# Kernel optimization log

Hardware: AMD Instinct MI355X
Metric: run time of the kernel (lower is better)

## Reference

```python
import jax, jax.numpy as jnp
import numpy as np

C = 256
CI = C // 2  # inter_channel = 128
B, H, W = 8, 64, 64


def setup_inputs() -> dict:
    key = jax.random.key(0)
    ks = jax.random.split(key, 9)
    s = 0.02
    return {
        "x": jax.random.normal(ks[0], (B, C, H, W), jnp.float32),
        "w_phi": jax.random.normal(ks[1], (CI, C), jnp.float32) * s,
        "b_phi": jax.random.normal(ks[2], (CI,), jnp.float32) * s,
        "w_theta": jax.random.normal(ks[3], (CI, C), jnp.float32) * s,
        "b_theta": jax.random.normal(ks[4], (CI,), jnp.float32) * s,
        "w_g": jax.random.normal(ks[5], (CI, C), jnp.float32) * s,
        "b_g": jax.random.normal(ks[6], (CI,), jnp.float32) * s,
        "w_mask": jax.random.normal(ks[7], (C, CI), jnp.float32) * s,
        "b_mask": jax.random.normal(ks[8], (C,), jnp.float32) * s,
    }


def reference(x, w_phi, b_phi, w_theta, b_theta, w_g, b_g, w_mask, b_mask):
    b, c, h, w = x.shape
    n = h * w
    xf = x.reshape(b, c, n)  # [b, c, n]
    # 1x1 convs == per-position channel projections
    phi = jnp.einsum('dc,bcn->bdn', w_phi, xf) + b_phi[:, None]      # [b, ci, n]
    theta = jnp.einsum('dc,bcn->bnd', w_theta, xf) + b_theta[None, None, :]  # [b, n, ci]
    g = jnp.einsum('dc,bcn->bnd', w_g, xf) + b_g[None, None, :]      # [b, n, ci]
    # full self-attention over spatial positions (no scaling, as in source)
    scores = jnp.einsum('bnd,bdm->bnm', theta, phi)                  # [b, n, n]
    attn = jax.nn.softmax(scores, axis=-1)
    y = jnp.einsum('bnm,bmd->bnd', attn, g)                          # [b, n, ci]
    # mask conv (1x1) back to channel dim + residual
    mask = jnp.einsum('cd,bnd->bcn', w_mask, y) + b_mask[:, None]    # [b, c, n]
    return mask.reshape(b, c, h, w) + x
```

## Files before the change

### kernel.cpp

```cpp
#include <hip/hip_runtime.h>

#define BB 8
#define CC 256
#define DD 128
#define NN 4096

#define LOG2E 1.44269504f
#define MSHIFT 32.0f

typedef __attribute__((ext_vector_type(8))) short short8;
typedef __attribute__((ext_vector_type(4))) short short4v;
typedef __attribute__((ext_vector_type(4))) float f32x4;
typedef __attribute__((ext_vector_type(16))) float f32x16;
typedef __attribute__((ext_vector_type(4))) unsigned int u32x4;

static __device__ __forceinline__ unsigned short f2bf(float f) {
    unsigned u = __builtin_bit_cast(unsigned, f);
    u += 0x7FFFu + ((u >> 16) & 1u);
    return (unsigned short)(u >> 16);
}
static __device__ __forceinline__ float bf2f(unsigned short h) {
    unsigned u = ((unsigned)h) << 16;
    return __builtin_bit_cast(float, u);
}
static __device__ __forceinline__ short8 pack8(float4 a, float4 b) {
    short8 r;
    r[0] = (short)f2bf(a.x); r[1] = (short)f2bf(a.y);
    r[2] = (short)f2bf(a.z); r[3] = (short)f2bf(a.w);
    r[4] = (short)f2bf(b.x); r[5] = (short)f2bf(b.y);
    r[6] = (short)f2bf(b.z); r[7] = (short)f2bf(b.w);
    return r;
}
static __device__ __forceinline__ unsigned cvtpk_bf16(float lo, float hi) {
    unsigned r;
    asm("v_cvt_pk_bf16_f32 %0, %1, %2" : "=v"(r) : "v"(lo), "v"(hi));
    return r;
}
static __device__ __forceinline__ void pl32swap(unsigned &a, unsigned &b) {
#if __has_builtin(__builtin_amdgcn_permlane32_swap)
    auto r = __builtin_amdgcn_permlane32_swap((int)a, (int)b, false, false);
    a = (unsigned)r[0]; b = (unsigned)r[1];
#else
    asm("v_permlane32_swap_b32 %0, %1" : "+v"(a), "+v"(b));
#endif
}

__global__ __launch_bounds__(256) void k_transpose_x(
        const float* __restrict__ x, unsigned short* __restrict__ xT) {
    __shared__ __align__(16) unsigned short tile[64][66];
    int nb = blockIdx.x * 64, cb = blockIdx.y * 64, b = blockIdx.z;
    const float* xp = x + (size_t)b * CC * NN;
    int t = threadIdx.x;
#pragma unroll
    for (int i = 0; i < 2; i++) {
        int idx = t + 256 * i;
        int c_l = idx >> 3;
        int n0 = (idx & 7) * 8;
        const float* src = xp + (size_t)(cb + c_l) * NN + nb + n0;
        float4 v0 = *(const float4*)(src);
        float4 v1 = *(const float4*)(src + 4);
        tile[n0 + 0][c_l] = f2bf(v0.x);
        tile[n0 + 1][c_l] = f2bf(v0.y);
        tile[n0 + 2][c_l] = f2bf(v0.z);
        tile[n0 + 3][c_l] = f2bf(v0.w);
        tile[n0 + 4][c_l] = f2bf(v1.x);
        tile[n0 + 5][c_l] = f2bf(v1.y);
        tile[n0 + 6][c_l] = f2bf(v1.z);
        tile[n0 + 7][c_l] = f2bf(v1.w);
    }
    __syncthreads();
    unsigned short* xtp = xT + (size_t)b * NN * CC;
#pragma unroll
    for (int i = 0; i < 2; i++) {
        int idx = t + 256 * i;
        int n_l = idx >> 3;
        int c0 = (idx & 7) * 8;
        const unsigned int* row = (const unsigned int*)&tile[n_l][0];
        uint4 o;
        o.x = row[(c0 >> 1) + 0];
        o.y = row[(c0 >> 1) + 1];
        o.z = row[(c0 >> 1) + 2];
        o.w = row[(c0 >> 1) + 3];
        *(uint4*)(xtp + (size_t)(nb + n_l) * CC + cb + c0) = o;
    }
}

__global__ __launch_bounds__(256) void k_proj(
        const unsigned short* __restrict__ xT,
        const float* __restrict__ w_phi, const float* __restrict__ b_phi,
        const float* __restrict__ w_theta, const float* __restrict__ b_theta,
        const float* __restrict__ w_g, const float* __restrict__ b_g,
        unsigned short* __restrict__ qws, unsigned short* __restrict__ kws,
        unsigned short* __restrict__ vtws) {
    __shared__ __align__(16) unsigned short xs[128][72];
    __shared__ __align__(16) unsigned short rp[128][136];
    int nb = blockIdx.x * 128, proj = blockIdx.y, b = blockIdx.z;
    const float *W, *bias;
    if (proj == 0) { W = w_theta; bias = b_theta; }
    else if (proj == 1) { W = w_phi; bias = b_phi; }
    else { W = w_g; bias = b_g; }
    float scl = (proj == 0) ? LOG2E : 1.0f;
    int t = threadIdx.x, lane = t & 63, wave = t >> 6;
    int l16 = lane & 15, l4 = lane >> 4;

    f32x4 acc[2][8];
#pragma unroll
    for (int mf = 0; mf < 2; mf++)
#pragma unroll
        for (int nf = 0; nf < 8; nf++)
#pragma unroll
            for (int e = 0; e < 4; e++) acc[mf][nf][e] = 0.f;

    const unsigned short* xtp = xT + (size_t)b * NN * CC;
    for (int kc = 0; kc < 4; kc++) {
        int c0k = kc * 64;
        __syncthreads();
#pragma unroll
        for (int i = 0; i < 4; i++) {
            int idx = t + 256 * i;
            int n = idx >> 3, cc = (idx & 7) * 8;
            *(short8*)&xs[n][cc] = *(const short8*)(xtp + (size_t)(nb + n) * CC + c0k + cc);
        }
        __syncthreads();
        short8 af[2][2];
#pragma unroll
        for (int mf = 0; mf < 2; mf++)
#pragma unroll
            for (int ic = 0; ic < 2; ic++) {
                int d = wave * 32 + mf * 16 + l16;
                const float* wp = W + d * CC + c0k + ic * 32 + l4 * 8;
                af[mf][ic] = pack8(*(const float4*)wp, *(const float4*)(wp + 4));
            }
#pragma unroll
        for (int nf = 0; nf < 8; nf++)
#pragma unroll
            for (int ic = 0; ic < 2; ic++) {
                short8 bfr = *(const short8*)&xs[nf * 16 + l16][ic * 32 + l4 * 8];
                acc[0][nf] = __builtin_amdgcn_mfma_f32_16x16x32_bf16(af[0][ic], bfr, acc[0][nf], 0, 0, 0);
                acc[1][nf] = __builtin_amdgcn_mfma_f32_16x16x32_bf16(af[1][ic], bfr, acc[1][nf], 0, 0, 0);
            }
    }
    __syncthreads();
    if (proj < 2) {
        unsigned short* outp = (proj == 0 ? qws : kws) + (size_t)b * NN * DD;
#pragma unroll
        for (int mf = 0; mf < 2; mf++) {
            int d0 = wave * 32 + mf * 16 + l4 * 4;
            float bb[4];
#pragma unroll
            for (int r = 0; r < 4; r++) bb[r] = bias[d0 + r];
#pragma unroll
            for (int nf = 0; nf < 8; nf++) {
                short4v pk;
#pragma unroll
                for (int r = 0; r < 4; r++) pk[r] = (short)f2bf((acc[mf][nf][r] + bb[r]) * scl);
                *(short4v*)&rp[nf * 16 + l16][d0] = pk;
            }
        }
        __syncthreads();
#pragma unroll
        for (int i = 0; i < 8; i++) {
            int idx = t + 256 * i;
            int n = idx >> 4, dd = (idx & 15) * 8;
            *(short8*)(outp + (size_t)(nb + n) * DD + dd) = *(const short8*)&rp[n][dd];
        }
    } else {
#pragma unroll
        for (int mf = 0; mf < 2; mf++) {
            int drow = wave * 32 + mf * 16 + l4 * 4;
            float bb[4];
#pragma unroll
            for (int r = 0; r < 4; r++) bb[r] = bias[drow + r];
#pragma unroll
            for (int nf = 0; nf < 8; nf++)
#pragma unroll
                for (int r = 0; r < 4; r++)
                    rp[drow + r][nf * 16 + l16] = f2bf(acc[mf][nf][r] + bb[r]);
        }
        __syncthreads();
        unsigned short* outp = vtws + (size_t)b * DD * NN;
#pragma unroll
        for (int i = 0; i < 8; i++) {
            int idx = t + 256 * i;
            int d = idx >> 4, n0 = (idx & 15) * 8;
            *(short8*)(outp + (size_t)d * NN + nb + n0) = *(const short8*)&rp[d][n0];
        }
    }
}

__global__ __launch_bounds__(128, 2) void k_flash(
        const unsigned short* __restrict__ q, const unsigned short* __restrict__ kk,
        const unsigned short* __restrict__ vt, unsigned short* __restrict__ opart,
        float* __restrict__ lsums) {
    __shared__ __align__(16) unsigned char smem[32768];

    int bid = blockIdx.x;
    int b   = bid & 7;
    int rem = bid >> 3;
    int ks  = rem >> 6;
    int qt  = rem & 63;
    int qb  = qt * 64;

    int t = threadIdx.x, lane = t & 63, wave = t >> 6;
    int l31 = lane & 31, hi = lane >> 5;

    const unsigned short* qp = q  + (size_t)b * NN * DD;
    const unsigned short* kp = kk + (size_t)b * NN * DD;
    const unsigned short* vp = vt + (size_t)b * DD * NN;

    short8 qreg[8];
    {
        int qrow = qb + wave * 32 + l31;
#pragma unroll
        for (int kc = 0; kc < 8; kc++)
            qreg[kc] = *(const short8*)(qp + (size_t)qrow * DD + kc * 16 + hi * 8);
    }

    f32x16 o[4];
#pragma unroll
    for (int df = 0; df < 4; df++)
#pragma unroll
        for (int e = 0; e < 16; e++) o[df][e] = 0.f;
    float lsum0 = 0.f, lsum1 = 0.f;

    int kbase = ks * (NN / 2);
    const int NIT = (NN / 2) / 32;

    {
        uint4 k0[4], v0[4];
#pragma unroll
        for (int i = 0; i < 4; i++) {
            int idx = t + 128 * i;
            k0[i] = *(const uint4*)(kp + (size_t)(kbase + (idx >> 4)) * DD + (idx & 15) * 8);
            v0[i] = *(const uint4*)(vp + (size_t)(idx >> 2) * NN + kbase + (idx & 3) * 8);
        }
#pragma unroll
        for (int i = 0; i < 4; i++) {
            int idx = t + 128 * i;
            int rk = idx >> 4, ck = idx & 15;
            *(uint4*)((char*)smem + rk * 256 + ((ck ^ (rk & 7)) << 4)) = k0[i];
            int rv = idx >> 2, cv = idx & 3;
            *(uint4*)((char*)smem + 16384 + rv * 64 + ((cv ^ ((rv ^ (rv >> 2)) & 3)) << 4)) = v0[i];
        }
    }
    __syncthreads();

    for (int it = 0; it < NIT; ++it) {
        char* Kb  = (char*)smem + (it & 1) * 8192;
        char* Vb  = (char*)smem + 16384 + (it & 1) * 8192;
        char* Kb2 = (char*)smem + ((it & 1) ^ 1) * 8192;
        char* Vb2 = (char*)smem + 16384 + (((it & 1) ^ 1)) * 8192;

        uint4 kreg[4], vreg[4];
        bool pf = (it + 1 < NIT);
        if (pf) {
            int mb2 = kbase + (it + 1) * 32;
#pragma unroll
            for (int i = 0; i < 4; i++) {
                int idx = t + 128 * i;
                kreg[i] = *(const uint4*)(kp + (size_t)(mb2 + (idx >> 4)) * DD + (idx & 15) * 8);
                vreg[i] = *(const uint4*)(vp + (size_t)(idx >> 2) * NN + mb2 + (idx & 3) * 8);
            }
        }

        f32x16 sA, sB;
#pragma unroll
        for (int e = 0; e < 16; e++) { sA[e] = -MSHIFT; sB[e] = 0.f; }
        __builtin_amdgcn_s_setprio(1);
#pragma unroll
        for (int kc = 0; kc < 8; kc += 2) {
            short8 a0 = *(const short8*)(Kb + l31 * 256 + ((((kc << 1) | hi) ^ (l31 & 7)) << 4));
            short8 a1 = *(const short8*)(Kb + l31 * 256 + (((((kc + 1) << 1) | hi) ^ (l31 & 7)) << 4));
            sA = __builtin_amdgcn_mfma_f32_32x32x16_bf16(a0, qreg[kc], sA, 0, 0, 0);
            sB = __builtin_amdgcn_mfma_f32_32x32x16_bf16(a1, qreg[kc + 1], sB, 0, 0, 0);
        }
        __builtin_amdgcn_s_setprio(0);

        u32x4 pa[2];
        {
            float p[16];
#pragma unroll
            for (int r = 0; r < 16; r++) {
                p[r] = __builtin_exp2f(sA[r] + sB[r]);
                if (r & 1) lsum1 += p[r]; else lsum0 += p[r];
            }
#pragma unroll
            for (int h = 0; h < 2; h++) {
                unsigned a0 = cvtpk_bf16(p[8 * h + 0], p[8 * h + 1]);
                unsigned a1 = cvtpk_bf16(p[8 * h + 2], p[8 * h + 3]);
                unsigned b0 = cvtpk_bf16(p[8 * h + 4], p[8 * h + 5]);
                unsigned b1 = cvtpk_bf16(p[8 * h + 6], p[8 * h + 7]);
                pl32swap(a0, b0);
                pl32swap(a1, b1);
                u32x4 v; v[0] = a0; v[1] = a1; v[2] = b0; v[3] = b1;
                pa[h] = v;
            }
        }

        __builtin_amdgcn_s_setprio(1);
#pragma unroll
        for (int df = 0; df < 4; df++) {
            int row = df * 32 + l31;
            int sw = (row ^ (row >> 2)) & 3;
#pragma unroll
            for (int c = 0; c < 2; c++) {
                short8 vb = *(const short8*)(Vb + row * 64 + ((((c << 1) | hi) ^ sw) << 4));
                o[df] = __builtin_amdgcn_mfma_f32_32x32x16_bf16(
                    __builtin_bit_cast(short8, pa[c]), vb, o[df], 0, 0, 0);
            }
        }
        __builtin_amdgcn_s_setprio(0);

        if (pf) {
#pragma unroll
            for (int i = 0; i < 4; i++) {
                int idx = t + 128 * i;
                int rk = idx >> 4, ck = idx & 15;
                *(uint4*)(Kb2 + rk * 256 + ((ck ^ (rk & 7)) << 4)) = kreg[i];
                int rv = idx >> 2, cv = idx & 3;
                *(uint4*)(Vb2 + rv * 64 + ((cv ^ ((rv ^ (rv >> 2)) & 3)) << 4)) = vreg[i];
            }
        }
        __syncthreads();
    }

    {
        float lsum = lsum0 + lsum1;
        float tot = lsum + __shfl_xor(lsum, 32);
        if (lane < 32)
            lsums[((size_t)ks * BB + b) * NN + qb + wave * 32 + l31] = tot;
    }
    unsigned short (*Ox)[136] = (unsigned short (*)[136])smem;
#pragma unroll
    for (int df = 0; df < 4; df++)
#pragma unroll
        for (int r = 0; r < 16; r++) {
            int qr = (r & 3) + 8 * (r >> 2) + 4 * hi;
            Ox[wave * 32 + qr][df * 32 + l31] = f2bf(o[df][r]);
        }
    __syncthreads();
    unsigned short* op = opart + (((size_t)ks * BB + b) * NN + qb) * DD;
#pragma unroll
    for (int i = 0; i < 8; i++) {
        int idx = t + 128 * i;
        int nr = idx >> 4, c0 = (idx & 15) * 8;
        *(short8*)(op + (size_t)nr * DD + c0) = *(const short8*)&Ox[nr][c0];
    }
}

__global__ __launch_bounds__(256) void k_maskout(
        const unsigned short* __restrict__ opart, const float* __restrict__ lsums,
        const float* __restrict__ w_mask, const float* __restrict__ b_mask,
        const float* __restrict__ x, float* __restrict__ out) {
    __shared__ __align__(16) unsigned short Ys[64][136];
    __shared__ float invl[64];
    int nb = blockIdx.x * 64, cs = blockIdx.y, b = blockIdx.z;
    int t = threadIdx.x, lane = t & 63, wave = t >> 6;
    int l16 = lane & 15, l4 = lane >> 4;

    const unsigned short* o0 = opart + ((size_t)b * NN + nb) * DD;
    const unsigned short* o1 = opart + (((size_t)BB + b) * NN + nb) * DD;
    if (t < 64) {
        float ls0 = lsums[(size_t)b * NN + nb + t];
        float ls1 = lsums[((size_t)BB + b) * NN + nb + t];
        invl[t] = 1.0f / (ls0 + ls1);
    }
    __syncthreads();
#pragma unroll
    for (int i = 0; i < 4; i++) {
        int idx = t + 256 * i;
        int nr = idx >> 4, d0 = (idx & 15) * 8;
        short8 a = *(const short8*)(o0 + (size_t)nr * DD + d0);
        short8 c = *(const short8*)(o1 + (size_t)nr * DD + d0);
        float inv = invl[nr];
        short8 yv;
#pragma unroll
        for (int j = 0; j < 8; j++)
            yv[j] = (short)f2bf((bf2f((unsigned short)a[j]) + bf2f((unsigned short)c[j])) * inv);
        *(short8*)&Ys[nr][d0] = yv;
    }
    __syncthreads();

    f32x4 acc[2][4];
#pragma unroll
    for (int mf = 0; mf < 2; mf++)
#pragma unroll
        for (int nf = 0; nf < 4; nf++)
#pragma unroll
            for (int e = 0; e < 4; e++) acc[mf][nf][e] = 0.f;

#pragma unroll
    for (int kc = 0; kc < 4; kc++) {
        int d0 = kc * 32 + l4 * 8;
        short8 af[2];
#pragma unroll
        for (int mf = 0; mf < 2; mf++) {
            int c = cs * 128 + wave * 32 + mf * 16 + l16;
            const float* wp = w_mask + c * DD + d0;
            af[mf] = pack8(*(const float4*)wp, *(const float4*)(wp + 4));
        }
#pragma unroll
        for (int nf = 0; nf < 4; nf++) {
            short8 bfr = *(const short8*)&Ys[nf * 16 + l16][d0];
#pragma unroll
            for (int mf = 0; mf < 2; mf++)
                acc[mf][nf] = __builtin_amdgcn_mfma_f32_16x16x32_bf16(af[mf], bfr, acc[mf][nf], 0, 0, 0);
        }
    }

    const float* xp = x + (size_t)b * CC * NN;
    float* op = out + (size_t)b * CC * NN;
#pragma unroll
    for (int mf = 0; mf < 2; mf++) {
        int c0 = cs * 128 + wave * 32 + mf * 16 + l4 * 4;
        float bb[4];
#pragma unroll
        for (int r = 0; r < 4; r++) bb[r] = b_mask[c0 + r];
#pragma unroll
        for (int r = 0; r < 4; r++) {
            size_t rowoff = (size_t)(c0 + r) * NN;
#pragma unroll
            for (int nf = 0; nf < 4; nf++) {
                int n = nb + nf * 16 + l16;
                op[rowoff + n] = acc[mf][nf][r] + bb[r] + xp[rowoff + n];
            }
        }
    }
}

extern "C" void kernel_launch(void* const* d_in, const int* in_sizes, int n_in,
                              void* d_out, int out_size, void* d_ws, size_t ws_size,
                              hipStream_t stream) {
    const float* x       = (const float*)d_in[0];
    const float* w_phi   = (const float*)d_in[1];
    const float* b_phi   = (const float*)d_in[2];
    const float* w_theta = (const float*)d_in[3];
    const float* b_theta = (const float*)d_in[4];
    const float* w_g     = (const float*)d_in[5];
    const float* b_g     = (const float*)d_in[6];
    const float* w_mask  = (const float*)d_in[7];
    const float* b_mask  = (const float*)d_in[8];
    float* out = (float*)d_out;

    char* ws = (char*)d_ws;
    unsigned short* xT    = (unsigned short*)(ws);
    unsigned short* opart = (unsigned short*)(ws);
    unsigned short* qw    = (unsigned short*)(ws + ((size_t)16 << 20));
    unsigned short* kw    = (unsigned short*)(ws + ((size_t)24 << 20));
    unsigned short* vtw   = (unsigned short*)(ws + ((size_t)32 << 20));
    float*          lsums = (float*)(ws + ((size_t)40 << 20));

    k_transpose_x<<<dim3(NN / 64, CC / 64, BB), 256, 0, stream>>>(x, xT);
    k_proj<<<dim3(NN / 128, 3, BB), 256, 0, stream>>>(xT, w_phi, b_phi, w_theta, b_theta,
                                                      w_g, b_g, qw, kw, vtw);
    k_flash<<<dim3(1024, 1, 1), 128, 0, stream>>>(qw, kw, vtw, opart, lsums);
    k_maskout<<<dim3(NN / 64, 2, BB), 256, 0, stream>>>(opart, lsums, w_mask, b_mask, x, out);
}
```

Before: 248.5 us.

## Software-pipeline QK^T of next tile with softmax/PV of current tile

Restructures the flash-attention inner loop so that the QK^T MFMAs for tile it+1 are interleaved with the exp2/bf16 packing of tile it, using two alternating score accumulators. Prefetch distance grows to two tiles, both K/V buffers are filled before the loop, and an extra barrier is added before each buffer overwrite. The aim is to overlap the transcendental/VALU softmax work with matrix-core work. In exchange it uses more registers and adds a second barrier per iteration. The final iteration computes scores for a nonexistent next tile from stale LDS, but those results are never used.

```diff
diff --git a/kernel.cpp b/kernel.cpp
--- a/kernel.cpp
+++ b/kernel.cpp
@@ -226,46 +226,34 @@
     int kbase = ks * (NN / 2);
     const int NIT = (NN / 2) / 32;
 
-    {
+#pragma unroll
+    for (int pt = 0; pt < 2; pt++) {
         uint4 k0[4], v0[4];
+        int mb = kbase + pt * 32;
 #pragma unroll
         for (int i = 0; i < 4; i++) {
             int idx = t + 128 * i;
-            k0[i] = *(const uint4*)(kp + (size_t)(kbase + (idx >> 4)) * DD + (idx & 15) * 8);
-            v0[i] = *(const uint4*)(vp + (size_t)(idx >> 2) * NN + kbase + (idx & 3) * 8);
-        }
+            k0[i] = *(const uint4*)(kp + (size_t)(mb + (idx >> 4)) * DD + (idx & 15) * 8);
+            v0[i] = *(const uint4*)(vp + (size_t)(idx >> 2) * NN + mb + (idx & 3) * 8);
+        }
+        char* Kb = (char*)smem + pt * 8192;
+        char* Vb = (char*)smem + 16384 + pt * 8192;
 #pragma unroll
         for (int i = 0; i < 4; i++) {
             int idx = t + 128 * i;
             int rk = idx >> 4, ck = idx & 15;
-            *(uint4*)((char*)smem + rk * 256 + ((ck ^ (rk & 7)) << 4)) = k0[i];
+            *(uint4*)(Kb + rk * 256 + ((ck ^ (rk & 7)) << 4)) = k0[i];
             int rv = idx >> 2, cv = idx & 3;
-            *(uint4*)((char*)smem + 16384 + rv * 64 + ((cv ^ ((rv ^ (rv >> 2)) & 3)) << 4)) = v0[i];
+            *(uint4*)(Vb + rv * 64 + ((cv ^ ((rv ^ (rv >> 2)) & 3)) << 4)) = v0[i];
         }
     }
     __syncthreads();
 
-    for (int it = 0; it < NIT; ++it) {
-        char* Kb  = (char*)smem + (it & 1) * 8192;
-        char* Vb  = (char*)smem + 16384 + (it & 1) * 8192;
-        char* Kb2 = (char*)smem + ((it & 1) ^ 1) * 8192;
-        char* Vb2 = (char*)smem + 16384 + (((it & 1) ^ 1)) * 8192;
-
-        uint4 kreg[4], vreg[4];
-        bool pf = (it + 1 < NIT);
-        if (pf) {
-            int mb2 = kbase + (it + 1) * 32;
-#pragma unroll
-            for (int i = 0; i < 4; i++) {
-                int idx = t + 128 * i;
-                kreg[i] = *(const uint4*)(kp + (size_t)(mb2 + (idx >> 4)) * DD + (idx & 15) * 8);
-                vreg[i] = *(const uint4*)(vp + (size_t)(idx >> 2) * NN + mb2 + (idx & 3) * 8);
-            }
-        }
-
-        f32x16 sA, sB;
-#pragma unroll
-        for (int e = 0; e < 16; e++) { sA[e] = -MSHIFT; sB[e] = 0.f; }
+    f32x16 sA, sB, sA2, sB2;
+#pragma unroll
+    for (int e = 0; e < 16; e++) { sA[e] = -MSHIFT; sB[e] = 0.f; }
+    {
+        char* Kb = (char*)smem;
         __builtin_amdgcn_s_setprio(1);
 #pragma unroll
         for (int kc = 0; kc < 8; kc += 2) {
@@ -275,29 +263,79 @@
             sB = __builtin_amdgcn_mfma_f32_32x32x16_bf16(a1, qreg[kc + 1], sB, 0, 0, 0);
         }
         __builtin_amdgcn_s_setprio(0);
-
+    }
+
+    auto body = [&](int it, f32x16& sAc, f32x16& sBc, f32x16& sAn, f32x16& sBn) {
+        char* KbN = (char*)smem + ((it + 1) & 1) * 8192;
+        char* Vb  = (char*)smem + 16384 + (it & 1) * 8192;
+        char* KbW = (char*)smem + (it & 1) * 8192;
+        char* VbW = (char*)smem + 16384 + (it & 1) * 8192;
+
+        uint4 kr[4], vr[4];
+        bool pf = (it + 2 < NIT);
+        if (pf) {
+            int mb2 = kbase + (it + 2) * 32;
+#pragma unroll
+            for (int i = 0; i < 4; i++) {
+                int idx = t + 128 * i;
+                kr[i] = *(const uint4*)(kp + (size_t)(mb2 + (idx >> 4)) * DD + (idx & 15) * 8);
+                vr[i] = *(const uint4*)(vp + (size_t)(idx >> 2) * NN + mb2 + (idx & 3) * 8);
+            }
+        }
+
+#pragma unroll
+        for (int e = 0; e < 16; e++) { sAn[e] = -MSHIFT; sBn[e] = 0.f; }
+
+        float p[16];
         u32x4 pa[2];
+        __builtin_amdgcn_s_setprio(1);
+#pragma unroll
+        for (int g = 0; g < 2; g++) {
+#pragma unroll
+            for (int r = 4 * g; r < 4 * g + 4; r++) {
+                p[r] = __builtin_exp2f(sAc[r] + sBc[r]);
+                if (r & 1) lsum1 += p[r]; else lsum0 += p[r];
+            }
+            int kc = 2 * g;
+            short8 a0 = *(const short8*)(KbN + l31 * 256 + ((((kc << 1) | hi) ^ (l31 & 7)) << 4));
+            short8 a1 = *(const short8*)(KbN + l31 * 256 + (((((kc + 1) << 1) | hi) ^ (l31 & 7)) << 4));
+            sAn = __builtin_amdgcn_mfma_f32_32x32x16_bf16(a0, qreg[kc], sAn, 0, 0, 0);
+            sBn = __builtin_amdgcn_mfma_f32_32x32x16_bf16(a1, qreg[kc + 1], sBn, 0, 0, 0);
+        }
         {
-            float p[16];
-#pragma unroll
-            for (int r = 0; r < 16; r++) {
-                p[r] = __builtin_exp2f(sA[r] + sB[r]);
+            unsigned a0 = cvtpk_bf16(p[0], p[1]);
+            unsigned a1 = cvtpk_bf16(p[2], p[3]);
+            unsigned b0 = cvtpk_bf16(p[4], p[5]);
+            unsigned b1 = cvtpk_bf16(p[6], p[7]);
+            pl32swap(a0, b0);
+            pl32swap(a1, b1);
+            u32x4 v; v[0] = a0; v[1] = a1; v[2] = b0; v[3] = b1;
+            pa[0] = v;
+        }
+#pragma unroll
+        for (int g = 2; g < 4; g++) {
+#pragma unroll
+            for (int r = 4 * g; r < 4 * g + 4; r++) {
+                p[r] = __builtin_exp2f(sAc[r] + sBc[r]);
                 if (r & 1) lsum1 += p[r]; else lsum0 += p[r];
             }
-#pragma unroll
-            for (int h = 0; h < 2; h++) {
-                unsigned a0 = cvtpk_bf16(p[8 * h + 0], p[8 * h + 1]);
-                unsigned a1 = cvtpk_bf16(p[8 * h + 2], p[8 * h + 3]);
-                unsigned b0 = cvtpk_bf16(p[8 * h + 4], p[8 * h + 5]);
-                unsigned b1 = cvtpk_bf16(p[8 * h + 6], p[8 * h + 7]);
-                pl32swap(a0, b0);
-                pl32swap(a1, b1);
-                u32x4 v; v[0] = a0; v[1] = a1; v[2] = b0; v[3] = b1;
-                pa[h] = v;
-            }
-        }
-
-        __builtin_amdgcn_s_setprio(1);
+            int kc = 2 * g;
+            short8 a0 = *(const short8*)(KbN + l31 * 256 + ((((kc << 1) | hi) ^ (l31 & 7)) << 4));
+            short8 a1 = *(const short8*)(KbN + l31 * 256 + (((((kc + 1) << 1) | hi) ^ (l31 & 7)) << 4));
+            sAn = __builtin_amdgcn_mfma_f32_32x32x16_bf16(a0, qreg[kc], sAn, 0, 0, 0);
+            sBn = __builtin_amdgcn_mfma_f32_32x32x16_bf16(a1, qreg[kc + 1], sBn, 0, 0, 0);
+        }
+        {
+            unsigned a0 = cvtpk_bf16(p[8], p[9]);
+            unsigned a1 = cvtpk_bf16(p[10], p[11]);
+            unsigned b0 = cvtpk_bf16(p[12], p[13]);
+            unsigned b1 = cvtpk_bf16(p[14], p[15]);
+            pl32swap(a0, b0);
+            pl32swap(a1, b1);
+            u32x4 v; v[0] = a0; v[1] = a1; v[2] = b0; v[3] = b1;
+            pa[1] = v;
+        }
+
 #pragma unroll
         for (int df = 0; df < 4; df++) {
             int row = df * 32 + l31;
@@ -311,17 +349,23 @@
         }
         __builtin_amdgcn_s_setprio(0);
 
+        __syncthreads();
         if (pf) {
 #pragma unroll
             for (int i = 0; i < 4; i++) {
                 int idx = t + 128 * i;
                 int rk = idx >> 4, ck = idx & 15;
-                *(uint4*)(Kb2 + rk * 256 + ((ck ^ (rk & 7)) << 4)) = kreg[i];
+                *(uint4*)(KbW + rk * 256 + ((ck ^ (rk & 7)) << 4)) = kr[i];
                 int rv = idx >> 2, cv = idx & 3;
-                *(uint4*)(Vb2 + rv * 64 + ((cv ^ ((rv ^ (rv >> 2)) & 3)) << 4)) = vreg[i];
+                *(uint4*)(VbW + rv * 64 + ((cv ^ ((rv ^ (rv >> 2)) & 3)) << 4)) = vr[i];
             }
         }
         __syncthreads();
+    };
+
+    for (int it = 0; it < NIT; it += 2) {
+        body(it, sA, sB, sA2, sB2);
+        body(it + 1, sA2, sB2, sA, sB);
     }
 
     {
```

Measured after the change: 426.6 us. 71.7% more time.

## Software-pipeline QK^T of next tile with softmax and PV of current tile

Applied to the files above, without the earlier changes.

Restructures the flash-attention inner loop so that the QK^T MFMAs for tile it+1 are interleaved with the exp2/softmax and PV MFMAs of tile it, using ping-pong score registers and a two-tile-ahead prefetch. The prologue loads two K/V tiles, and the loop is unrolled by two with macros. The split sA/sB score accumulation is collapsed into a single chain. The aim is to hide transcendental and conversion latency behind matrix-core work, at the cost of more registers, an extra barrier per iteration, and more complex buffer indexing.

```diff
diff --git a/kernel.cpp b/kernel.cpp
--- a/kernel.cpp
+++ b/kernel.cpp
@@ -188,6 +188,82 @@
     }
 }
 
+#define KFRAG(BUF, KC) \
+    (*(const short8*)((BUF) + l31 * 256 + (((((KC) << 1) | hi) ^ (l31 & 7)) << 4)))
+
+#define QGROUP(SC, SN, KBN, G, P0, P1, P2, P3)                                        \
+    P0 = __builtin_exp2f(SC[4 * (G) + 0]); lsum0 += P0;                               \
+    P1 = __builtin_exp2f(SC[4 * (G) + 1]); lsum1 += P1;                               \
+    P2 = __builtin_exp2f(SC[4 * (G) + 2]); lsum0 += P2;                               \
+    P3 = __builtin_exp2f(SC[4 * (G) + 3]); lsum1 += P3;                               \
+    SN = __builtin_amdgcn_mfma_f32_32x32x16_bf16(KFRAG(KBN, 2 * (G)), qreg[2 * (G)], SN, 0, 0, 0); \
+    SN = __builtin_amdgcn_mfma_f32_32x32x16_bf16(KFRAG(KBN, 2 * (G) + 1), qreg[2 * (G) + 1], SN, 0, 0, 0);
+
+#define PABUILD(PA, Pa, Pb, Pc, Pd, Pe, Pf_, Pg, Ph) {                                \
+    unsigned x0 = cvtpk_bf16(Pa, Pb);                                                 \
+    unsigned x1 = cvtpk_bf16(Pc, Pd);                                                 \
+    unsigned y0 = cvtpk_bf16(Pe, Pf_);                                                \
+    unsigned y1 = cvtpk_bf16(Pg, Ph);                                                 \
+    pl32swap(x0, y0); pl32swap(x1, y1);                                               \
+    PA[0] = x0; PA[1] = x1; PA[2] = y0; PA[3] = y1; }
+
+#define PVSTEP(DF, PA0, PA1) {                                                        \
+    int row_ = (DF) * 32 + l31;                                                       \
+    int sw_ = (row_ ^ (row_ >> 2)) & 3;                                               \
+    short8 vb0 = *(const short8*)(Vb + row_ * 64 + (((0 | hi) ^ sw_) << 4));          \
+    short8 vb1 = *(const short8*)(Vb + row_ * 64 + (((2 | hi) ^ sw_) << 4));          \
+    o[DF] = __builtin_amdgcn_mfma_f32_32x32x16_bf16(                                  \
+        __builtin_bit_cast(short8, PA0), vb0, o[DF], 0, 0, 0);                        \
+    o[DF] = __builtin_amdgcn_mfma_f32_32x32x16_bf16(                                  \
+        __builtin_bit_cast(short8, PA1), vb1, o[DF], 0, 0, 0); }
+
+#define FLASH_BODY(ITC, PAR, SC, SN) {                                                \
+    char* KbN = (char*)smem + ((PAR) ^ 1) * 8192;                                     \
+    char* Vb  = (char*)smem + 16384 + (PAR) * 8192;                                   \
+    char* KbW = (char*)smem + (PAR) * 8192;                                           \
+    char* VbW = (char*)smem + 16384 + (PAR) * 8192;                                   \
+    uint4 kr0, kr1, kr2, kr3, vr0, vr1, vr2, vr3;                                     \
+    bool pf = ((ITC) + 2 < NIT);                                                      \
+    if (pf) {                                                                         \
+        int mb2 = kbase + ((ITC) + 2) * 32;                                           \
+        int i0 = t, i1 = t + 128, i2 = t + 256, i3 = t + 384;                         \
+        kr0 = *(const uint4*)(kp + (size_t)(mb2 + (i0 >> 4)) * DD + (i0 & 15) * 8);   \
+        kr1 = *(const uint4*)(kp + (size_t)(mb2 + (i1 >> 4)) * DD + (i1 & 15) * 8);   \
+        kr2 = *(const uint4*)(kp + (size_t)(mb2 + (i2 >> 4)) * DD + (i2 & 15) * 8);   \
+        kr3 = *(const uint4*)(kp + (size_t)(mb2 + (i3 >> 4)) * DD + (i3 & 15) * 8);   \
+        vr0 = *(const uint4*)(vp + (size_t)(i0 >> 2) * NN + mb2 + (i0 & 3) * 8);      \
+        vr1 = *(const uint4*)(vp + (size_t)(i1 >> 2) * NN + mb2 + (i1 & 3) * 8);      \
+        vr2 = *(const uint4*)(vp + (size_t)(i2 >> 2) * NN + mb2 + (i2 & 3) * 8);      \
+        vr3 = *(const uint4*)(vp + (size_t)(i3 >> 2) * NN + mb2 + (i3 & 3) * 8);      \
+    }                                                                                 \
+    _Pragma("unroll") for (int e = 0; e < 16; e++) SN[e] = -MSHIFT;                   \
+    float p0, p1, p2, p3, p4, p5, p6, p7, p8, p9, p10, p11, p12, p13, p14, p15;       \
+    __builtin_amdgcn_s_setprio(1);                                                    \
+    QGROUP(SC, SN, KbN, 0, p0, p1, p2, p3)                                            \
+    QGROUP(SC, SN, KbN, 1, p4, p5, p6, p7)                                            \
+    u32x4 paA; PABUILD(paA, p0, p1, p2, p3, p4, p5, p6, p7)                           \
+    QGROUP(SC, SN, KbN, 2, p8, p9, p10, p11)                                          \
+    QGROUP(SC, SN, KbN, 3, p12, p13, p14, p15)                                        \
+    u32x4 paB; PABUILD(paB, p8, p9, p10, p11, p12, p13, p14, p15)                     \
+    PVSTEP(0, paA, paB)                                                               \
+    PVSTEP(1, paA, paB)                                                               \
+    PVSTEP(2, paA, paB)                                                               \
+    PVSTEP(3, paA, paB)                                                               \
+    __builtin_amdgcn_s_setprio(0);                                                    \
+    __syncthreads();                                                                  \
+    if (pf) {                                                                         \
+        int i0 = t, i1 = t + 128, i2 = t + 256, i3 = t + 384;                         \
+        *(uint4*)(KbW + (i0 >> 4) * 256 + (((i0 & 15) ^ ((i0 >> 4) & 7)) << 4)) = kr0; \
+        *(uint4*)(KbW + (i1 >> 4) * 256 + (((i1 & 15) ^ ((i1 >> 4) & 7)) << 4)) = kr1; \
+        *(uint4*)(KbW + (i2 >> 4) * 256 + (((i2 & 15) ^ ((i2 >> 4) & 7)) << 4)) = kr2; \
+        *(uint4*)(KbW + (i3 >> 4) * 256 + (((i3 & 15) ^ ((i3 >> 4) & 7)) << 4)) = kr3; \
+        *(uint4*)(VbW + (i0 >> 2) * 64 + ((((i0 & 3) ^ (((i0 >> 2) ^ (i0 >> 4)) & 3)) << 4))) = vr0; \
+        *(uint4*)(VbW + (i1 >> 2) * 64 + ((((i1 & 3) ^ (((i1 >> 2) ^ (i1 >> 4)) & 3)) << 4))) = vr1; \
+        *(uint4*)(VbW + (i2 >> 2) * 64 + ((((i2 & 3) ^ (((i2 >> 2) ^ (i2 >> 4)) & 3)) << 4))) = vr2; \
+        *(uint4*)(VbW + (i3 >> 2) * 64 + ((((i3 & 3) ^ (((i3 >> 2) ^ (i3 >> 4)) & 3)) << 4))) = vr3; \
+    }                                                                                 \
+    __syncthreads(); }
+
 __global__ __launch_bounds__(128, 2) void k_flash(
         const unsigned short* __restrict__ q, const unsigned short* __restrict__ kk,
         const unsigned short* __restrict__ vt, unsigned short* __restrict__ opart,
@@ -226,102 +302,44 @@
     int kbase = ks * (NN / 2);
     const int NIT = (NN / 2) / 32;
 
-    {
+#pragma unroll
+    for (int pt = 0; pt < 2; pt++) {
         uint4 k0[4], v0[4];
+        int mb = kbase + pt * 32;
 #pragma unroll
         for (int i = 0; i < 4; i++) {
             int idx = t + 128 * i;
-            k0[i] = *(const uint4*)(kp + (size_t)(kbase + (idx >> 4)) * DD + (idx & 15) * 8);
-            v0[i] = *(const uint4*)(vp + (size_t)(idx >> 2) * NN + kbase + (idx & 3) * 8);
-        }
+            k0[i] = *(const uint4*)(kp + (size_t)(mb + (idx >> 4)) * DD + (idx & 15) * 8);
+            v0[i] = *(const uint4*)(vp + (size_t)(idx >> 2) * NN + mb + (idx & 3) * 8);
+        }
+        char* Kb = (char*)smem + pt * 8192;
+        char* Vb = (char*)smem + 16384 + pt * 8192;
 #pragma unroll
         for (int i = 0; i < 4; i++) {
             int idx = t + 128 * i;
             int rk = idx >> 4, ck = idx & 15;
-            *(uint4*)((char*)smem + rk * 256 + ((ck ^ (rk & 7)) << 4)) = k0[i];
+            *(uint4*)(Kb + rk * 256 + ((ck ^ (rk & 7)) << 4)) = k0[i];
             int rv = idx >> 2, cv = idx & 3;
-            *(uint4*)((char*)smem + 16384 + rv * 64 + ((cv ^ ((rv ^ (rv >> 2)) & 3)) << 4)) = v0[i];
-        }
-    }
-    __syncthreads();
-
-    for (int it = 0; it < NIT; ++it) {
-        char* Kb  = (char*)smem + (it & 1) * 8192;
-        char* Vb  = (char*)smem + 16384 + (it & 1) * 8192;
-        char* Kb2 = (char*)smem + ((it & 1) ^ 1) * 8192;
-        char* Vb2 = (char*)smem + 16384 + (((it & 1) ^ 1)) * 8192;
-
-        uint4 kreg[4], vreg[4];
-        bool pf = (it + 1 < NIT);
-        if (pf) {
-            int mb2 = kbase + (it + 1) * 32;
-#pragma unroll
-            for (int i = 0; i < 4; i++) {
-                int idx = t + 128 * i;
-                kreg[i] = *(const uint4*)(kp + (size_t)(mb2 + (idx >> 4)) * DD + (idx & 15) * 8);
-                vreg[i] = *(const uint4*)(vp + (size_t)(idx >> 2) * NN + mb2 + (idx & 3) * 8);
-            }
-        }
-
-        f32x16 sA, sB;
-#pragma unroll
-        for (int e = 0; e < 16; e++) { sA[e] = -MSHIFT; sB[e] = 0.f; }
+            *(uint4*)(Vb + rv * 64 + ((cv ^ ((rv ^ (rv >> 2)) & 3)) << 4)) = v0[i];
+        }
+    }
+    __syncthreads();
+
+    f32x16 s0, s1;
+#pragma unroll
+    for (int e = 0; e < 16; e++) s0[e] = -MSHIFT;
+    {
+        char* Kb0 = (char*)smem;
         __builtin_amdgcn_s_setprio(1);
 #pragma unroll
-        for (int kc = 0; kc < 8; kc += 2) {
-            short8 a0 = *(const short8*)(Kb + l31 * 256 + ((((kc << 1) | hi) ^ (l31 & 7)) << 4));
-            short8 a1 = *(const short8*)(Kb + l31 * 256 + (((((kc + 1) << 1) | hi) ^ (l31 & 7)) << 4));
-            sA = __builtin_amdgcn_mfma_f32_32x32x16_bf16(a0, qreg[kc], sA, 0, 0, 0);
-            sB = __builtin_amdgcn_mfma_f32_32x32x16_bf16(a1, qreg[kc + 1], sB, 0, 0, 0);
-        }
+        for (int kc = 0; kc < 8; kc++)
+            s0 = __builtin_amdgcn_mfma_f32_32x32x16_bf16(KFRAG(Kb0, kc), qreg[kc], s0, 0, 0, 0);
         __builtin_amdgcn_s_setprio(0);
-
-        u32x4 pa[2];
-        {
-            float p[16];
-#pragma unroll
-            for (int r = 0; r < 16; r++) {
-                p[r] = __builtin_exp2f(sA[r] + sB[r]);
-                if (r & 1) lsum1 += p[r]; else lsum0 += p[r];
-            }
-#pragma unroll
-            for (int h = 0; h < 2; h++) {
-                unsigned a0 = cvtpk_bf16(p[8 * h + 0], p[8 * h + 1]);
-                unsigned a1 = cvtpk_bf16(p[8 * h + 2], p[8 * h + 3]);
-                unsigned b0 = cvtpk_bf16(p[8 * h + 4], p[8 * h + 5]);
-                unsigned b1 = cvtpk_bf16(p[8 * h + 6], p[8 * h + 7]);
-                pl32swap(a0, b0);
-                pl32swap(a1, b1);
-                u32x4 v; v[0] = a0; v[1] = a1; v[2] = b0; v[3] = b1;
-                pa[h] = v;
-            }
-        }
-
-        __builtin_amdgcn_s_setprio(1);
-#pragma unroll
-        for (int df = 0; df < 4; df++) {
-            int row = df * 32 + l31;
-            int sw = (row ^ (row >> 2)) & 3;
-#pragma unroll
-            for (int c = 0; c < 2; c++) {
-                short8 vb = *(const short8*)(Vb + row * 64 + ((((c << 1) | hi) ^ sw) << 4));
-                o[df] = __builtin_amdgcn_mfma_f32_32x32x16_bf16(
-                    __builtin_bit_cast(short8, pa[c]), vb, o[df], 0, 0, 0);
-            }
-        }
-        __builtin_amdgcn_s_setprio(0);
-
-        if (pf) {
-#pragma unroll
-            for (int i = 0; i < 4; i++) {
-                int idx = t + 128 * i;
-                int rk = idx >> 4, ck = idx & 15;
-                *(uint4*)(Kb2 + rk * 256 + ((ck ^ (rk & 7)) << 4)) = kreg[i];
-                int rv = idx >> 2, cv = idx & 3;
-                *(uint4*)(Vb2 + rv * 64 + ((cv ^ ((rv ^ (rv >> 2)) & 3)) << 4)) = vreg[i];
-            }
-        }
-        __syncthreads();
+    }
+
+    for (int it = 0; it < NIT; it += 2) {
+        FLASH_BODY(it, 0, s0, s1)
+        FLASH_BODY(it + 1, 1, s1, s0)
     }
 
     {
```

Result: slower. 295.2 us (+18.8%).

## Fuse x transpose into projection kernel and coalesce mask-output epilogue via LDS

Applied to the files above, without the earlier changes.

Removes the separate transpose kernel: k_proj now reads fp32 x directly, converts it to bf16 and transposes it into LDS with an XOR-style swizzle to avoid bank conflicts. This drops one launch and the bf16 xT round trip through global memory, but x is now read three times, once per projection. The mask kernel epilogue stages its results in LDS so the residual add and output store use coalesced float4 accesses instead of scattered scalar ones.

```diff
diff --git a/kernel.cpp b/kernel.cpp
--- a/kernel.cpp
+++ b/kernel.cpp
@@ -45,48 +45,8 @@
 #endif
 }
 
-__global__ __launch_bounds__(256) void k_transpose_x(
-        const float* __restrict__ x, unsigned short* __restrict__ xT) {
-    __shared__ __align__(16) unsigned short tile[64][66];
-    int nb = blockIdx.x * 64, cb = blockIdx.y * 64, b = blockIdx.z;
-    const float* xp = x + (size_t)b * CC * NN;
-    int t = threadIdx.x;
-#pragma unroll
-    for (int i = 0; i < 2; i++) {
-        int idx = t + 256 * i;
-        int c_l = idx >> 3;
-        int n0 = (idx & 7) * 8;
-        const float* src = xp + (size_t)(cb + c_l) * NN + nb + n0;
-        float4 v0 = *(const float4*)(src);
-        float4 v1 = *(const float4*)(src + 4);
-        tile[n0 + 0][c_l] = f2bf(v0.x);
-        tile[n0 + 1][c_l] = f2bf(v0.y);
-        tile[n0 + 2][c_l] = f2bf(v0.z);
-        tile[n0 + 3][c_l] = f2bf(v0.w);
-        tile[n0 + 4][c_l] = f2bf(v1.x);
-        tile[n0 + 5][c_l] = f2bf(v1.y);
-        tile[n0 + 6][c_l] = f2bf(v1.z);
-        tile[n0 + 7][c_l] = f2bf(v1.w);
-    }
-    __syncthreads();
-    unsigned short* xtp = xT + (size_t)b * NN * CC;
-#pragma unroll
-    for (int i = 0; i < 2; i++) {
-        int idx = t + 256 * i;
-        int n_l = idx >> 3;
-        int c0 = (idx & 7) * 8;
-        const unsigned int* row = (const unsigned int*)&tile[n_l][0];
-        uint4 o;
-        o.x = row[(c0 >> 1) + 0];
-        o.y = row[(c0 >> 1) + 1];
-        o.z = row[(c0 >> 1) + 2];
-        o.w = row[(c0 >> 1) + 3];
-        *(uint4*)(xtp + (size_t)(nb + n_l) * CC + cb + c0) = o;
-    }
-}
-
 __global__ __launch_bounds__(256) void k_proj(
-        const unsigned short* __restrict__ xT,
+        const float* __restrict__ x,
         const float* __restrict__ w_phi, const float* __restrict__ b_phi,
         const float* __restrict__ w_theta, const float* __restrict__ b_theta,
         const float* __restrict__ w_g, const float* __restrict__ b_g,
@@ -111,15 +71,27 @@
 #pragma unroll
             for (int e = 0; e < 4; e++) acc[mf][nf][e] = 0.f;
 
-    const unsigned short* xtp = xT + (size_t)b * NN * CC;
+    const float* xpb = x + (size_t)b * CC * NN;
+    int cl = t >> 2;
+    int gq = t & 3;
+    int n0 = gq * 32;
+    int wcol = (cl + 16 * gq) & 63;
+
     for (int kc = 0; kc < 4; kc++) {
         int c0k = kc * 64;
         __syncthreads();
-#pragma unroll
-        for (int i = 0; i < 4; i++) {
-            int idx = t + 256 * i;
-            int n = idx >> 3, cc = (idx & 7) * 8;
-            *(short8*)&xs[n][cc] = *(const short8*)(xtp + (size_t)(nb + n) * CC + c0k + cc);
+        {
+            const float* src = xpb + (size_t)(c0k + cl) * NN + nb + n0;
+            float4 xv[8];
+#pragma unroll
+            for (int j = 0; j < 8; j++) xv[j] = *(const float4*)(src + 4 * j);
+#pragma unroll
+            for (int j = 0; j < 8; j++) {
+                xs[n0 + 4 * j + 0][wcol] = f2bf(xv[j].x);
+                xs[n0 + 4 * j + 1][wcol] = f2bf(xv[j].y);
+                xs[n0 + 4 * j + 2][wcol] = f2bf(xv[j].z);
+                xs[n0 + 4 * j + 3][wcol] = f2bf(xv[j].w);
+            }
         }
         __syncthreads();
         short8 af[2][2];
@@ -135,7 +107,8 @@
         for (int nf = 0; nf < 8; nf++)
 #pragma unroll
             for (int ic = 0; ic < 2; ic++) {
-                short8 bfr = *(const short8*)&xs[nf * 16 + l16][ic * 32 + l4 * 8];
+                int rcol = (ic * 32 + l4 * 8 + 16 * (nf >> 1)) & 63;
+                short8 bfr = *(const short8*)&xs[nf * 16 + l16][rcol];
                 acc[0][nf] = __builtin_amdgcn_mfma_f32_16x16x32_bf16(af[0][ic], bfr, acc[0][nf], 0, 0, 0);
                 acc[1][nf] = __builtin_amdgcn_mfma_f32_16x16x32_bf16(af[1][ic], bfr, acc[1][nf], 0, 0, 0);
             }
@@ -182,8 +155,8 @@
 #pragma unroll
         for (int i = 0; i < 8; i++) {
             int idx = t + 256 * i;
-            int d = idx >> 4, n0 = (idx & 15) * 8;
-            *(short8*)(outp + (size_t)d * NN + nb + n0) = *(const short8*)&rp[d][n0];
+            int d = idx >> 4, n0s = (idx & 15) * 8;
+            *(short8*)(outp + (size_t)d * NN + nb + n0s) = *(const short8*)&rp[d][n0s];
         }
     }
 }
@@ -352,8 +325,10 @@
         const unsigned short* __restrict__ opart, const float* __restrict__ lsums,
         const float* __restrict__ w_mask, const float* __restrict__ b_mask,
         const float* __restrict__ x, float* __restrict__ out) {
-    __shared__ __align__(16) unsigned short Ys[64][136];
-    __shared__ float invl[64];
+    __shared__ __align__(16) unsigned char pool[35072];
+    unsigned short (*Ys)[136] = (unsigned short (*)[136])pool;
+    float (*Os)[68] = (float (*)[68])pool;
+    float* invl = (float*)(pool + 34816);
     int nb = blockIdx.x * 64, cs = blockIdx.y, b = blockIdx.z;
     int t = threadIdx.x, lane = t & 63, wave = t >> 6;
     int l16 = lane & 15, l4 = lane >> 4;
@@ -407,24 +382,34 @@
                 acc[mf][nf] = __builtin_amdgcn_mfma_f32_16x16x32_bf16(af[mf], bfr, acc[mf][nf], 0, 0, 0);
         }
     }
-
-    const float* xp = x + (size_t)b * CC * NN;
-    float* op = out + (size_t)b * CC * NN;
+    __syncthreads();
+
 #pragma unroll
     for (int mf = 0; mf < 2; mf++) {
-        int c0 = cs * 128 + wave * 32 + mf * 16 + l4 * 4;
+        int c0 = wave * 32 + mf * 16 + l4 * 4;
         float bb[4];
 #pragma unroll
-        for (int r = 0; r < 4; r++) bb[r] = b_mask[c0 + r];
-#pragma unroll
-        for (int r = 0; r < 4; r++) {
-            size_t rowoff = (size_t)(c0 + r) * NN;
-#pragma unroll
-            for (int nf = 0; nf < 4; nf++) {
-                int n = nb + nf * 16 + l16;
-                op[rowoff + n] = acc[mf][nf][r] + bb[r] + xp[rowoff + n];
-            }
-        }
+        for (int r = 0; r < 4; r++) bb[r] = b_mask[cs * 128 + c0 + r];
+#pragma unroll
+        for (int r = 0; r < 4; r++)
+#pragma unroll
+            for (int nf = 0; nf < 4; nf++)
+                Os[c0 + r][nf * 16 + l16] = acc[mf][nf][r] + bb[r];
+    }
+    __syncthreads();
+
+    const float* xp = x + (size_t)b * CC * NN + (size_t)cs * 128 * NN + nb;
+    float* op = out + (size_t)b * CC * NN + (size_t)cs * 128 * NN + nb;
+#pragma unroll
+    for (int i = 0; i < 8; i++) {
+        int idx = t + 256 * i;
+        int c = idx >> 4, nq = (idx & 15) * 4;
+        float4 osv = *(const float4*)&Os[c][nq];
+        float4 xv = *(const float4*)(xp + (size_t)c * NN + nq);
+        float4 ov;
+        ov.x = osv.x + xv.x; ov.y = osv.y + xv.y;
+        ov.z = osv.z + xv.z; ov.w = osv.w + xv.w;
+        *(float4*)(op + (size_t)c * NN + nq) = ov;
     }
 }
 
@@ -443,15 +428,13 @@
     float* out = (float*)d_out;
 
     char* ws = (char*)d_ws;
-    unsigned short* xT    = (unsigned short*)(ws);
     unsigned short* opart = (unsigned short*)(ws);
     unsigned short* qw    = (unsigned short*)(ws + ((size_t)16 << 20));
     unsigned short* kw    = (unsigned short*)(ws + ((size_t)24 << 20));
     unsigned short* vtw   = (unsigned short*)(ws + ((size_t)32 << 20));
     float*          lsums = (float*)(ws + ((size_t)40 << 20));
 
-    k_transpose_x<<<dim3(NN / 64, CC / 64, BB), 256, 0, stream>>>(x, xT);
-    k_proj<<<dim3(NN / 128, 3, BB), 256, 0, stream>>>(xT, w_phi, b_phi, w_theta, b_theta,
+    k_proj<<<dim3(NN / 128, 3, BB), 256, 0, stream>>>(x, w_phi, b_phi, w_theta, b_theta,
                                                       w_g, b_g, qw, kw, vtw);
     k_flash<<<dim3(1024, 1, 1), 128, 0, stream>>>(qw, kw, vtw, opart, lsums);
     k_maskout<<<dim3(NN / 64, 2, BB), 256, 0, stream>>>(opart, lsums, w_mask, b_mask, x, out);
```

Result: faster. 233.4 us (-6.1%).
